# Kernel optimization log

Measured on AMD Instinct MI355X. Metric: run time of the kernel, lower is better.

The kernel has to match this reference:

```python
import jax, jax.numpy as jnp
import numpy as np

D_MODEL, D_STATE, D_CONV, D_INNER, DT_RANK = 1024, 16, 4, 2048, 64
B_SZ, L = 4, 2048

def setup_inputs() -> dict:
    key = jax.random.key(0)
    ks = jax.random.split(key, 7)
    return {
        "hidden_states": jax.random.normal(ks[0], (B_SZ, L, D_MODEL), jnp.float32),
        "in_proj_w": jax.random.normal(ks[1], (2 * D_INNER, D_MODEL), jnp.float32) * (D_MODEL ** -0.5),
        "conv_w": jax.random.normal(ks[2], (D_INNER, 1, D_CONV), jnp.float32) * 0.5,
        "conv_b": jax.random.normal(ks[3], (D_INNER,), jnp.float32) * 0.1,
        "x_proj_w": jax.random.normal(ks[4], (DT_RANK + 2 * D_STATE, D_INNER), jnp.float32) * (D_INNER ** -0.5),
        "dt_proj_w": jax.random.normal(ks[5], (D_INNER, DT_RANK), jnp.float32) * (DT_RANK ** -0.5),
        "A_log": jax.random.uniform(ks[6], (D_INNER, D_STATE), jnp.float32, 0.0, 2.0),
    }

def reference(hidden_states, in_proj_w, conv_w, conv_b, x_proj_w, dt_proj_w, A_log):
    b, l, d = hidden_states.shape
    # in_proj: (b,l,d) x (2*d_inner,d)^T -> (b, 2*d_inner, l)
    xz = jnp.einsum('bld,ed->bel', hidden_states, in_proj_w)
    x, z = jnp.split(xz, 2, axis=1)  # each (b, d_inner, l); z unused downstream
    A = -jnp.exp(A_log)              # (d_inner, d_state)
    # causal depthwise conv1d (left pad d_conv-1) + SiLU
    x = jax.lax.conv_general_dilated(
        x, conv_w, window_strides=(1,), padding=[(D_CONV - 1, 0)],
        feature_group_count=D_INNER,
        dimension_numbers=('NCH', 'OIH', 'NCH'))
    x = jax.nn.silu(x + conv_b[None, :, None])  # (b, d_inner, l)
    # x_proj: (b,l,dt_rank+2*d_state)
    x_dbl = jnp.einsum('bdl,ed->ble', x, x_proj_w)
    dt, B_mat, C_mat = jnp.split(x_dbl, [DT_RANK, DT_RANK + D_STATE], axis=-1)
    dt = jnp.einsum('blr,dr->bdl', dt, dt_proj_w)          # (b, d_inner, l), no bias
    B_mat = jnp.swapaxes(B_mat, 1, 2)                      # (b, d_state, l)
    C_mat = jnp.swapaxes(C_mat, 1, 2)                      # (b, d_state, l)
    return (dt, A, B_mat, C_mat, x)
```

## Files before the change

kernel.cpp:

```cpp
#include <hip/hip_runtime.h>
#include <hip/hip_bf16.h>
#include <math.h>

#define D_MODEL 1024
#define D_STATE 16
#define D_CONV  4
#define D_INNER 2048
#define DT_RANK 64
#define B_SZ    4
#define L_SEQ   2048

#define OFF_DT 0
#define OFF_A  (B_SZ * D_INNER * L_SEQ)
#define OFF_B  (OFF_A + D_INNER * D_STATE)
#define OFF_C  (OFF_B + B_SZ * D_STATE * L_SEQ)
#define OFF_X  (OFF_C + B_SZ * D_STATE * L_SEQ)

typedef __attribute__((ext_vector_type(8))) short bf16x8;
typedef __attribute__((ext_vector_type(8))) unsigned short us8;
typedef __attribute__((ext_vector_type(4))) float f32x4;
typedef unsigned short ushort_t;
typedef unsigned int uint_t;

static __device__ __forceinline__ ushort_t f2bf(float f) {
  __hip_bfloat16 h = __float2bfloat16(f);
  return *(ushort_t*)&h;
}
static __device__ __forceinline__ float bf2f(ushort_t u) {
  union { uint_t u; float f; } c;
  c.u = ((uint_t)u) << 16;
  return c.f;
}

#define N4_HS   (B_SZ * L_SEQ * D_MODEL / 4)
#define N4_W    (D_INNER * D_MODEL / 4)
#define N4_XW   ((DT_RANK + 2 * D_STATE) * D_INNER / 4)
#define N4_Z0   (B_SZ * DT_RANK * L_SEQ / 4)
#define N4_Z1   (2 * B_SZ * D_STATE * L_SEQ / 4)
#define N4_A    (D_INNER * D_STATE / 4)
#define N4_TOT  (N4_HS + N4_W + N4_XW + N4_Z0 + N4_Z1 + N4_A)

__global__ __launch_bounds__(256) void k_prep(
    const float4* __restrict__ hs, const float4* __restrict__ ipw,
    const float4* __restrict__ xpw, const float4* __restrict__ alog,
    ushort4* __restrict__ bfHS, ushort4* __restrict__ bfW,
    ushort4* __restrict__ xwb,
    float4* __restrict__ z0, float4* __restrict__ z1,
    float4* __restrict__ aout) {
  int i = blockIdx.x * 256 + threadIdx.x;
  if (i < N4_HS) {
    float4 v = hs[i];
    ushort4 o; o.x = f2bf(v.x); o.y = f2bf(v.y); o.z = f2bf(v.z); o.w = f2bf(v.w);
    bfHS[i] = o;
    return;
  }
  i -= N4_HS;
  if (i < N4_W) {
    float4 v = ipw[i];
    ushort4 o; o.x = f2bf(v.x); o.y = f2bf(v.y); o.z = f2bf(v.z); o.w = f2bf(v.w);
    bfW[i] = o;
    return;
  }
  i -= N4_W;
  if (i < N4_XW) {
    float4 v = xpw[i];
    ushort4 o; o.x = f2bf(v.x); o.y = f2bf(v.y); o.z = f2bf(v.z); o.w = f2bf(v.w);
    xwb[i] = o;
    return;
  }
  i -= N4_XW;
  if (i < N4_Z0) { z0[i] = (float4){0.f, 0.f, 0.f, 0.f}; return; }
  i -= N4_Z0;
  if (i < N4_Z1) { z1[i] = (float4){0.f, 0.f, 0.f, 0.f}; return; }
  i -= N4_Z1;
  if (i < N4_A) {
    float4 v = alog[i];
    float4 o;
    o.x = -expf(v.x); o.y = -expf(v.y); o.z = -expf(v.z); o.w = -expf(v.w);
    aout[i] = o;
  }
}

__global__ __launch_bounds__(256) void k_inproj_mfma(
    const ushort_t* __restrict__ Wb,
    const ushort_t* __restrict__ HSb,
    ushort_t* __restrict__ Cout) {
  const int flat = blockIdx.x + 16 * blockIdx.y + 256 * blockIdx.z;
  const int swz  = (flat & 7) * 128 + (flat >> 3);
  const int bn = swz & 15;
  const int bm = (swz >> 4) & 15;
  const int b  = swz >> 8;

  __shared__ ushort_t As[128 * 32];
  __shared__ ushort_t Bs[128 * 32];
  const int tid  = threadIdx.x;
  const int wv   = tid >> 6;
  const int lane = tid & 63;
  const int wr = wv >> 1, wc = wv & 1;

  const int srow = tid >> 2;
  const int ss   = tid & 3;

  const ushort_t* Ag = Wb + (size_t)(bm * 128) * D_MODEL;
  const ushort_t* Bg = HSb + (size_t)b * L_SEQ * D_MODEL
                           + (size_t)(bn * 128) * D_MODEL;

  f32x4 acc[4][4];
#pragma unroll
  for (int i = 0; i < 4; ++i)
#pragma unroll
    for (int j = 0; j < 4; ++j) acc[i][j] = (f32x4){0.f, 0.f, 0.f, 0.f};

  const int ksel = lane >> 4;
  const int frow = lane & 15;

  for (int k0 = 0; k0 < D_MODEL; k0 += 32) {
#pragma unroll
    for (int q = 0; q < 2; ++q) {
      int row = q * 64 + srow;
      int xs  = ss ^ ((row >> 1) & 3);
      const ushort_t* ga = Ag + (size_t)row * D_MODEL + k0 + xs * 8;
      const ushort_t* gb = Bg + (size_t)row * D_MODEL + k0 + xs * 8;
      ushort_t* la = As + (q * 256 + wv * 64) * 8;
      ushort_t* lb = Bs + (q * 256 + wv * 64) * 8;
      __builtin_amdgcn_global_load_lds((const __attribute__((address_space(1))) void*)ga,
                                       (__attribute__((address_space(3))) void*)la, 16, 0, 0);
      __builtin_amdgcn_global_load_lds((const __attribute__((address_space(1))) void*)gb,
                                       (__attribute__((address_space(3))) void*)lb, 16, 0, 0);
    }
    __syncthreads();

    bf16x8 af[4], bfr[4];
#pragma unroll
    for (int m = 0; m < 4; ++m) {
      int row = wr * 64 + m * 16 + frow;
      af[m] = *(const bf16x8*)(As + (row * 4 + (ksel ^ ((row >> 1) & 3))) * 8);
    }
#pragma unroll
    for (int n = 0; n < 4; ++n) {
      int row = wc * 64 + n * 16 + frow;
      bfr[n] = *(const bf16x8*)(Bs + (row * 4 + (ksel ^ ((row >> 1) & 3))) * 8);
    }
#pragma unroll
    for (int m = 0; m < 4; ++m)
#pragma unroll
      for (int n = 0; n < 4; ++n)
        acc[m][n] = __builtin_amdgcn_mfma_f32_16x16x32_bf16(af[m], bfr[n], acc[m][n], 0, 0, 0);
    __syncthreads();
  }

  const int crow0 = (lane >> 4) * 4;
  const int ccol  = lane & 15;
  ushort_t* Cb = Cout + (size_t)b * D_INNER * L_SEQ;
#pragma unroll
  for (int m = 0; m < 4; ++m) {
    int gr0 = bm * 128 + wr * 64 + m * 16 + crow0;
#pragma unroll
    for (int n = 0; n < 4; ++n) {
      int gc = bn * 128 + wc * 64 + n * 16 + ccol;
#pragma unroll
      for (int i = 0; i < 4; ++i)
        Cb[(size_t)(gr0 + i) * L_SEQ + gc] = f2bf(acc[m][n][i]);
    }
  }
}

__global__ __launch_bounds__(256) void k_conv(const ushort_t* __restrict__ Xp,
                                              const float* __restrict__ CW,
                                              const float* __restrict__ CB,
                                              float* __restrict__ Xo) {
  const int bd = blockIdx.x;
  const int d  = bd & (D_INNER - 1);
  const ushort_t* row = Xp + (size_t)bd * L_SEQ;
  float* orow = Xo + (size_t)bd * L_SEQ;
  const float w0 = CW[d * 4 + 0], w1 = CW[d * 4 + 1];
  const float w2 = CW[d * 4 + 2], w3 = CW[d * 4 + 3];
  const float bias = CB[d];
  const int l0 = threadIdx.x << 3;

  us8 cur = *(const us8*)(row + l0);
  float e[11];
  e[0] = 0.f; e[1] = 0.f; e[2] = 0.f;
  if (l0 >= 4) {
    ushort4 pv = *(const ushort4*)(row + l0 - 4);
    e[0] = bf2f(pv.y); e[1] = bf2f(pv.z); e[2] = bf2f(pv.w);
  }
#pragma unroll
  for (int j = 0; j < 8; ++j) e[3 + j] = bf2f(cur[j]);

  float4 o0, o1;
  float* op = &o0.x;
#pragma unroll
  for (int j = 0; j < 8; ++j) {
    float v = w0 * e[j] + w1 * e[j + 1] + w2 * e[j + 2] + w3 * e[j + 3] + bias;
    float s = v / (1.f + expf(-v));
    if (j < 4) (&o0.x)[j] = s; else (&o1.x)[j - 4] = s;
  }
  (void)op;
  *(float4*)(orow + l0)     = o0;
  *(float4*)(orow + l0 + 4) = o1;
}

__global__ __launch_bounds__(256) void k_xproj_mfma(
    const ushort_t* __restrict__ XWb,
    const float* __restrict__ X,
    float* __restrict__ XDBL,
    float* __restrict__ OutB,
    float* __restrict__ OutC) {
  const int ln = blockIdx.x;
  const int sk = blockIdx.y;
  const int b  = blockIdx.z;
  __shared__ ushort_t As[96 * 40];
  __shared__ ushort_t Bs[128 * 34];
  const int tid  = threadIdx.x;
  const int wv   = tid >> 6;
  const int lane = tid & 63;
  const int wr = wv >> 1, wc = wv & 1;
  const int ksel = lane >> 4;
  const int frow = lane & 15;

  const float* Xb = X + (size_t)b * D_INNER * L_SEQ + (size_t)ln * 128;

  f32x4 acc[3][4];
#pragma unroll
  for (int i = 0; i < 3; ++i)
#pragma unroll
    for (int j = 0; j < 4; ++j) acc[i][j] = (f32x4){0.f, 0.f, 0.f, 0.f};

  for (int k0 = 0; k0 < 256; k0 += 32) {
    const int koff = sk * 256 + k0;
    {
      int row = tid >> 2, s = tid & 3;
      bf16x8 v = *(const bf16x8*)(XWb + (size_t)row * D_INNER + koff + s * 8);
      *(bf16x8*)(As + row * 40 + s * 8) = v;
      if (tid < 128) {
        int row2 = 64 + (tid >> 2);
        bf16x8 v2 = *(const bf16x8*)(XWb + (size_t)row2 * D_INNER + koff + s * 8);
        *(bf16x8*)(As + row2 * 40 + s * 8) = v2;
      }
    }
#pragma unroll
    for (int j = 0; j < 2; ++j) {
      int u = tid + 256 * j;
      int n4 = u & 31;
      int kp = u >> 5;
      const float* g0 = Xb + (size_t)(koff + 2 * kp) * L_SEQ + 4 * n4;
      float4 x0 = *(const float4*)g0;
      float4 x1 = *(const float4*)(g0 + L_SEQ);
      float e0[4] = {x0.x, x0.y, x0.z, x0.w};
      float e1[4] = {x1.x, x1.y, x1.z, x1.w};
#pragma unroll
      for (int i = 0; i < 4; ++i) {
        uint_t pk = (uint_t)f2bf(e0[i]) | ((uint_t)f2bf(e1[i]) << 16);
        int n = 4 * n4 + i;
        *(uint_t*)(Bs + n * 34 + 2 * kp) = pk;
      }
    }
    __syncthreads();

    bf16x8 af[3], bfr[4];
#pragma unroll
    for (int mi = 0; mi < 3; ++mi) {
      int row = wr * 48 + mi * 16 + frow;
      af[mi] = *(const bf16x8*)(As + row * 40 + ksel * 8);
    }
#pragma unroll
    for (int ni = 0; ni < 4; ++ni) {
      int n = wc * 64 + ni * 16 + frow;
      const uint_t* p = (const uint_t*)(Bs + n * 34);
      union { uint_t u[4]; bf16x8 v; } fr;
#pragma unroll
      for (int q = 0; q < 4; ++q) fr.u[q] = p[ksel * 4 + q];
      bfr[ni] = fr.v;
    }
#pragma unroll
    for (int mi = 0; mi < 3; ++mi)
#pragma unroll
      for (int ni = 0; ni < 4; ++ni)
        acc[mi][ni] = __builtin_amdgcn_mfma_f32_16x16x32_bf16(af[mi], bfr[ni], acc[mi][ni], 0, 0, 0);
    __syncthreads();
  }

  const int crow0 = (lane >> 4) * 4;
  const int ccol  = lane & 15;
#pragma unroll
  for (int mi = 0; mi < 3; ++mi) {
    int e0 = wr * 48 + mi * 16 + crow0;
    float* base;
    int eoff;
    if (e0 < 64)      { base = XDBL + (size_t)b * 64 * L_SEQ; eoff = e0; }
    else if (e0 < 80) { base = OutB + (size_t)b * D_STATE * L_SEQ; eoff = e0 - 64; }
    else              { base = OutC + (size_t)b * D_STATE * L_SEQ; eoff = e0 - 80; }
#pragma unroll
    for (int ni = 0; ni < 4; ++ni) {
      int l = ln * 128 + wc * 64 + ni * 16 + ccol;
#pragma unroll
      for (int r = 0; r < 4; ++r)
        atomicAdd(base + (size_t)(eoff + r) * L_SEQ + l, acc[mi][ni][r]);
    }
  }
}

__global__ __launch_bounds__(256) void k_dt(const float* __restrict__ DW,
                                            const float* __restrict__ XDBL,
                                            float* __restrict__ DT) {
  const int b = blockIdx.z, bm = blockIdx.y, bn = blockIdx.x;
  __shared__ float As[64][68];
  __shared__ float Bs[64][68];
  const int tid = threadIdx.x;
  const int tx = tid & 15, ty = tid >> 4;
  const int row = tid >> 4;
  const int col = (tid & 15) << 2;
  const float* Bb = XDBL + (size_t)b * DT_RANK * L_SEQ;
#pragma unroll
  for (int q = 0; q < 4; ++q) {
    int r = q * 16 + row;
    float4 av = *(const float4*)(DW + (size_t)(bm * 64 + r) * DT_RANK + col);
    As[col + 0][r] = av.x; As[col + 1][r] = av.y;
    As[col + 2][r] = av.z; As[col + 3][r] = av.w;
    float4 bv = *(const float4*)(Bb + (size_t)r * L_SEQ + bn * 64 + col);
    *(float4*)&Bs[r][col] = bv;
  }
  __syncthreads();
  float acc[4][4] = {};
#pragma unroll 16
  for (int kk = 0; kk < 64; ++kk) {
    float4 a4 = *(const float4*)&As[kk][ty << 2];
    float4 b4 = *(const float4*)&Bs[kk][tx << 2];
    float a[4] = {a4.x, a4.y, a4.z, a4.w};
    float bb[4] = {b4.x, b4.y, b4.z, b4.w};
#pragma unroll
    for (int i = 0; i < 4; ++i)
#pragma unroll
      for (int j = 0; j < 4; ++j) acc[i][j] += a[i] * bb[j];
  }
  float* Cp = DT + (size_t)b * D_INNER * L_SEQ
                 + (size_t)(bm * 64 + (ty << 2)) * L_SEQ + bn * 64 + (tx << 2);
#pragma unroll
  for (int i = 0; i < 4; ++i) {
    float4 v = make_float4(acc[i][0], acc[i][1], acc[i][2], acc[i][3]);
    *(float4*)(Cp + (size_t)i * L_SEQ) = v;
  }
}

extern "C" void kernel_launch(void* const* d_in, const int* in_sizes, int n_in,
                              void* d_out, int out_size, void* d_ws, size_t ws_size,
                              hipStream_t stream) {
  const float* hs   = (const float*)d_in[0];
  const float* ipw  = (const float*)d_in[1];
  const float* cw   = (const float*)d_in[2];
  const float* cb   = (const float*)d_in[3];
  const float* xpw  = (const float*)d_in[4];
  const float* dpw  = (const float*)d_in[5];
  const float* alog = (const float*)d_in[6];

  float* out    = (float*)d_out;
  float* dt_out = out + OFF_DT;
  float* a_out  = out + OFF_A;
  float* b_out  = out + OFF_B;
  float* c_out  = out + OFF_C;
  float* x_out  = out + OFF_X;

  unsigned short* bfHS = (unsigned short*)x_out;
  unsigned short* bfW  = bfHS + (size_t)B_SZ * L_SEQ * D_MODEL;
  unsigned short* xpre = (unsigned short*)dt_out;
  float* xdbl = (float*)d_ws;
  unsigned short* xwb = (unsigned short*)((char*)d_ws + (size_t)B_SZ * DT_RANK * L_SEQ * 4);

  k_prep<<<dim3(N4_TOT / 256), 256, 0, stream>>>(
      (const float4*)hs, (const float4*)ipw, (const float4*)xpw,
      (const float4*)alog,
      (ushort4*)bfHS, (ushort4*)bfW, (ushort4*)xwb,
      (float4*)xdbl, (float4*)b_out, (float4*)a_out);

  k_inproj_mfma<<<dim3(16, 16, 4), 256, 0, stream>>>(bfW, bfHS, xpre);
  k_conv<<<dim3(B_SZ * D_INNER), 256, 0, stream>>>(xpre, cw, cb, x_out);
  k_xproj_mfma<<<dim3(16, 8, 4), 256, 0, stream>>>(xwb, x_out, xdbl, b_out, c_out);
  k_dt<<<dim3(32, 32, 4), 256, 0, stream>>>(dpw, xdbl, dt_out);
}
```

Measured before the change: 149.4 us.

## Fuse causal conv+SiLU into x_proj GEMM and move dt_proj to bf16 MFMA

The standalone conv kernel is removed. The x_proj GEMM now loads the bf16 pre-conv activations, applies the depthwise causal conv, bias and SiLU in its tile loader, writes the fp32 x output, and feeds the bf16 result straight into LDS. This avoids reading the full fp32 x tensor back and saves a launch. The fp32 SIMT dt_proj GEMM is replaced by a bf16 MFMA kernel on 128x128 tiles, with the weight converted to bf16 in the prep kernel. The trade-off is lower dt precision and scalar per-lane output stores in place of the earlier float4 stores.

```diff
diff --git a/kernel.cpp b/kernel.cpp
--- a/kernel.cpp
+++ b/kernel.cpp
@@ -35,16 +35,18 @@
 #define N4_HS   (B_SZ * L_SEQ * D_MODEL / 4)
 #define N4_W    (D_INNER * D_MODEL / 4)
 #define N4_XW   ((DT_RANK + 2 * D_STATE) * D_INNER / 4)
+#define N4_DW   (D_INNER * DT_RANK / 4)
 #define N4_Z0   (B_SZ * DT_RANK * L_SEQ / 4)
 #define N4_Z1   (2 * B_SZ * D_STATE * L_SEQ / 4)
 #define N4_A    (D_INNER * D_STATE / 4)
-#define N4_TOT  (N4_HS + N4_W + N4_XW + N4_Z0 + N4_Z1 + N4_A)
+#define N4_TOT  (N4_HS + N4_W + N4_XW + N4_DW + N4_Z0 + N4_Z1 + N4_A)
 
 __global__ __launch_bounds__(256) void k_prep(
     const float4* __restrict__ hs, const float4* __restrict__ ipw,
-    const float4* __restrict__ xpw, const float4* __restrict__ alog,
+    const float4* __restrict__ xpw, const float4* __restrict__ dpw,
+    const float4* __restrict__ alog,
     ushort4* __restrict__ bfHS, ushort4* __restrict__ bfW,
-    ushort4* __restrict__ xwb,
+    ushort4* __restrict__ xwb, ushort4* __restrict__ dwb,
     float4* __restrict__ z0, float4* __restrict__ z1,
     float4* __restrict__ aout) {
   int i = blockIdx.x * 256 + threadIdx.x;
@@ -69,6 +71,13 @@
     return;
   }
   i -= N4_XW;
+  if (i < N4_DW) {
+    float4 v = dpw[i];
+    ushort4 o; o.x = f2bf(v.x); o.y = f2bf(v.y); o.z = f2bf(v.z); o.w = f2bf(v.w);
+    dwb[i] = o;
+    return;
+  }
+  i -= N4_DW;
   if (i < N4_Z0) { z0[i] = (float4){0.f, 0.f, 0.f, 0.f}; return; }
   i -= N4_Z0;
   if (i < N4_Z1) { z1[i] = (float4){0.f, 0.f, 0.f, 0.f}; return; }
@@ -165,45 +174,12 @@
   }
 }
 
-__global__ __launch_bounds__(256) void k_conv(const ushort_t* __restrict__ Xp,
-                                              const float* __restrict__ CW,
-                                              const float* __restrict__ CB,
-                                              float* __restrict__ Xo) {
-  const int bd = blockIdx.x;
-  const int d  = bd & (D_INNER - 1);
-  const ushort_t* row = Xp + (size_t)bd * L_SEQ;
-  float* orow = Xo + (size_t)bd * L_SEQ;
-  const float w0 = CW[d * 4 + 0], w1 = CW[d * 4 + 1];
-  const float w2 = CW[d * 4 + 2], w3 = CW[d * 4 + 3];
-  const float bias = CB[d];
-  const int l0 = threadIdx.x << 3;
-
-  us8 cur = *(const us8*)(row + l0);
-  float e[11];
-  e[0] = 0.f; e[1] = 0.f; e[2] = 0.f;
-  if (l0 >= 4) {
-    ushort4 pv = *(const ushort4*)(row + l0 - 4);
-    e[0] = bf2f(pv.y); e[1] = bf2f(pv.z); e[2] = bf2f(pv.w);
-  }
-#pragma unroll
-  for (int j = 0; j < 8; ++j) e[3 + j] = bf2f(cur[j]);
-
-  float4 o0, o1;
-  float* op = &o0.x;
-#pragma unroll
-  for (int j = 0; j < 8; ++j) {
-    float v = w0 * e[j] + w1 * e[j + 1] + w2 * e[j + 2] + w3 * e[j + 3] + bias;
-    float s = v / (1.f + expf(-v));
-    if (j < 4) (&o0.x)[j] = s; else (&o1.x)[j - 4] = s;
-  }
-  (void)op;
-  *(float4*)(orow + l0)     = o0;
-  *(float4*)(orow + l0 + 4) = o1;
-}
-
-__global__ __launch_bounds__(256) void k_xproj_mfma(
+__global__ __launch_bounds__(256) void k_xproj_fused(
     const ushort_t* __restrict__ XWb,
-    const float* __restrict__ X,
+    const ushort_t* __restrict__ Xpre,
+    const float* __restrict__ CW,
+    const float* __restrict__ CB,
+    float* __restrict__ Xout,
     float* __restrict__ XDBL,
     float* __restrict__ OutB,
     float* __restrict__ OutC) {
@@ -219,8 +195,6 @@
   const int ksel = lane >> 4;
   const int frow = lane & 15;
 
-  const float* Xb = X + (size_t)b * D_INNER * L_SEQ + (size_t)ln * 128;
-
   f32x4 acc[3][4];
 #pragma unroll
   for (int i = 0; i < 3; ++i)
@@ -244,16 +218,33 @@
       int u = tid + 256 * j;
       int n4 = u & 31;
       int kp = u >> 5;
-      const float* g0 = Xb + (size_t)(koff + 2 * kp) * L_SEQ + 4 * n4;
-      float4 x0 = *(const float4*)g0;
-      float4 x1 = *(const float4*)(g0 + L_SEQ);
-      float e0[4] = {x0.x, x0.y, x0.z, x0.w};
-      float e1[4] = {x1.x, x1.y, x1.z, x1.w};
+      int l0 = ln * 128 + 4 * n4;
+      float sv[2][4];
+#pragma unroll
+      for (int r = 0; r < 2; ++r) {
+        int d = koff + 2 * kp + r;
+        const ushort_t* row = Xpre + ((size_t)b * D_INNER + d) * L_SEQ;
+        ushort4 cur = *(const ushort4*)(row + l0);
+        float em3 = 0.f, em2 = 0.f, em1 = 0.f;
+        if (l0 >= 4) {
+          ushort4 pv = *(const ushort4*)(row + l0 - 4);
+          em3 = bf2f(pv.y); em2 = bf2f(pv.z); em1 = bf2f(pv.w);
+        }
+        float ee[7] = {em3, em2, em1, bf2f(cur.x), bf2f(cur.y), bf2f(cur.z), bf2f(cur.w)};
+        float4 w = *(const float4*)(CW + d * 4);
+        float bias = CB[d];
+#pragma unroll
+        for (int i = 0; i < 4; ++i) {
+          float v = w.x * ee[i] + w.y * ee[i + 1] + w.z * ee[i + 2] + w.w * ee[i + 3] + bias;
+          sv[r][i] = v / (1.f + expf(-v));
+        }
+        *(float4*)(Xout + ((size_t)b * D_INNER + d) * L_SEQ + l0) =
+            make_float4(sv[r][0], sv[r][1], sv[r][2], sv[r][3]);
+      }
 #pragma unroll
       for (int i = 0; i < 4; ++i) {
-        uint_t pk = (uint_t)f2bf(e0[i]) | ((uint_t)f2bf(e1[i]) << 16);
-        int n = 4 * n4 + i;
-        *(uint_t*)(Bs + n * 34 + 2 * kp) = pk;
+        uint_t pk = (uint_t)f2bf(sv[0][i]) | ((uint_t)f2bf(sv[1][i]) << 16);
+        *(uint_t*)(Bs + (4 * n4 + i) * 34 + 2 * kp) = pk;
       }
     }
     __syncthreads();
@@ -301,45 +292,86 @@
   }
 }
 
-__global__ __launch_bounds__(256) void k_dt(const float* __restrict__ DW,
-                                            const float* __restrict__ XDBL,
-                                            float* __restrict__ DT) {
-  const int b = blockIdx.z, bm = blockIdx.y, bn = blockIdx.x;
-  __shared__ float As[64][68];
-  __shared__ float Bs[64][68];
-  const int tid = threadIdx.x;
-  const int tx = tid & 15, ty = tid >> 4;
-  const int row = tid >> 4;
-  const int col = (tid & 15) << 2;
-  const float* Bb = XDBL + (size_t)b * DT_RANK * L_SEQ;
+__global__ __launch_bounds__(256) void k_dt_mfma(
+    const ushort_t* __restrict__ DWb,
+    const float* __restrict__ XDBL,
+    float* __restrict__ DT) {
+  const int ln = blockIdx.x;
+  const int dm = blockIdx.y;
+  const int b  = blockIdx.z;
+  __shared__ ushort_t As[128 * 72];
+  __shared__ ushort_t Bs[128 * 68];
+  const int tid  = threadIdx.x;
+  const int wv   = tid >> 6;
+  const int lane = tid & 63;
+  const int wr = wv >> 1, wc = wv & 1;
+  const int ksel = lane >> 4;
+  const int frow = lane & 15;
+
 #pragma unroll
   for (int q = 0; q < 4; ++q) {
-    int r = q * 16 + row;
-    float4 av = *(const float4*)(DW + (size_t)(bm * 64 + r) * DT_RANK + col);
-    As[col + 0][r] = av.x; As[col + 1][r] = av.y;
-    As[col + 2][r] = av.z; As[col + 3][r] = av.w;
-    float4 bv = *(const float4*)(Bb + (size_t)r * L_SEQ + bn * 64 + col);
-    *(float4*)&Bs[r][col] = bv;
+    int u = tid + 256 * q;
+    int row = u >> 3, s = u & 7;
+    *(bf16x8*)(As + row * 72 + s * 8) =
+        *(const bf16x8*)(DWb + (size_t)(dm * 128 + row) * DT_RANK + s * 8);
+  }
+#pragma unroll
+  for (int q = 0; q < 4; ++q) {
+    int u = tid + 256 * q;
+    int n4 = u & 31;
+    int kp = u >> 5;
+    const float* g = XDBL + ((size_t)b * DT_RANK + 2 * kp) * L_SEQ + ln * 128 + 4 * n4;
+    float4 x0 = *(const float4*)g;
+    float4 x1 = *(const float4*)(g + L_SEQ);
+    float e0[4] = {x0.x, x0.y, x0.z, x0.w};
+    float e1[4] = {x1.x, x1.y, x1.z, x1.w};
+#pragma unroll
+    for (int i = 0; i < 4; ++i) {
+      uint_t pk = (uint_t)f2bf(e0[i]) | ((uint_t)f2bf(e1[i]) << 16);
+      *(uint_t*)(Bs + (4 * n4 + i) * 68 + 2 * kp) = pk;
+    }
   }
   __syncthreads();
-  float acc[4][4] = {};
-#pragma unroll 16
-  for (int kk = 0; kk < 64; ++kk) {
-    float4 a4 = *(const float4*)&As[kk][ty << 2];
-    float4 b4 = *(const float4*)&Bs[kk][tx << 2];
-    float a[4] = {a4.x, a4.y, a4.z, a4.w};
-    float bb[4] = {b4.x, b4.y, b4.z, b4.w};
-#pragma unroll
-    for (int i = 0; i < 4; ++i)
-#pragma unroll
-      for (int j = 0; j < 4; ++j) acc[i][j] += a[i] * bb[j];
-  }
-  float* Cp = DT + (size_t)b * D_INNER * L_SEQ
-                 + (size_t)(bm * 64 + (ty << 2)) * L_SEQ + bn * 64 + (tx << 2);
-#pragma unroll
-  for (int i = 0; i < 4; ++i) {
-    float4 v = make_float4(acc[i][0], acc[i][1], acc[i][2], acc[i][3]);
-    *(float4*)(Cp + (size_t)i * L_SEQ) = v;
+
+  f32x4 acc[4][4];
+#pragma unroll
+  for (int i = 0; i < 4; ++i)
+#pragma unroll
+    for (int j = 0; j < 4; ++j) acc[i][j] = (f32x4){0.f, 0.f, 0.f, 0.f};
+
+#pragma unroll
+  for (int ks = 0; ks < 2; ++ks) {
+    bf16x8 af[4], bfr[4];
+#pragma unroll
+    for (int m = 0; m < 4; ++m) {
+      int row = wr * 64 + m * 16 + frow;
+      af[m] = *(const bf16x8*)(As + row * 72 + ks * 32 + ksel * 8);
+    }
+#pragma unroll
+    for (int n = 0; n < 4; ++n) {
+      int nn = wc * 64 + n * 16 + frow;
+      bfr[n] = *(const bf16x8*)(Bs + nn * 68 + ks * 32 + ksel * 8);
+    }
+#pragma unroll
+    for (int m = 0; m < 4; ++m)
+#pragma unroll
+      for (int n = 0; n < 4; ++n)
+        acc[m][n] = __builtin_amdgcn_mfma_f32_16x16x32_bf16(af[m], bfr[n], acc[m][n], 0, 0, 0);
+  }
+
+  const int crow0 = (lane >> 4) * 4;
+  const int ccol  = lane & 15;
+  float* Cb = DT + (size_t)b * D_INNER * L_SEQ;
+#pragma unroll
+  for (int m = 0; m < 4; ++m) {
+    int gr0 = dm * 128 + wr * 64 + m * 16 + crow0;
+#pragma unroll
+    for (int n = 0; n < 4; ++n) {
+      int gc = ln * 128 + wc * 64 + n * 16 + ccol;
+#pragma unroll
+      for (int i = 0; i < 4; ++i)
+        Cb[(size_t)(gr0 + i) * L_SEQ + gc] = acc[m][n][i];
+    }
   }
 }
 
@@ -365,16 +397,17 @@
   unsigned short* bfW  = bfHS + (size_t)B_SZ * L_SEQ * D_MODEL;
   unsigned short* xpre = (unsigned short*)dt_out;
   float* xdbl = (float*)d_ws;
-  unsigned short* xwb = (unsigned short*)((char*)d_ws + (size_t)B_SZ * DT_RANK * L_SEQ * 4);
-
-  k_prep<<<dim3(N4_TOT / 256), 256, 0, stream>>>(
+  unsigned short* xwb = (unsigned short*)((char*)d_ws + 2097152);
+  unsigned short* dwb = (unsigned short*)((char*)d_ws + 2097152 + 393216);
+
+  k_prep<<<dim3((N4_TOT + 255) / 256), 256, 0, stream>>>(
       (const float4*)hs, (const float4*)ipw, (const float4*)xpw,
-      (const float4*)alog,
-      (ushort4*)bfHS, (ushort4*)bfW, (ushort4*)xwb,
+      (const float4*)dpw, (const float4*)alog,
+      (ushort4*)bfHS, (ushort4*)bfW, (ushort4*)xwb, (ushort4*)dwb,
       (float4*)xdbl, (float4*)b_out, (float4*)a_out);
 
   k_inproj_mfma<<<dim3(16, 16, 4), 256, 0, stream>>>(bfW, bfHS, xpre);
-  k_conv<<<dim3(B_SZ * D_INNER), 256, 0, stream>>>(xpre, cw, cb, x_out);
-  k_xproj_mfma<<<dim3(16, 8, 4), 256, 0, stream>>>(xwb, x_out, xdbl, b_out, c_out);
-  k_dt<<<dim3(32, 32, 4), 256, 0, stream>>>(dpw, xdbl, dt_out);
-}
+  k_xproj_fused<<<dim3(16, 8, 4), 256, 0, stream>>>(xwb, xpre, cw, cb,
+                                                    x_out, xdbl, b_out, c_out);
+  k_dt_mfma<<<dim3(16, 16, 4), 256, 0, stream>>>(dwb, xdbl, dt_out);
+}
```

Result: faster. 133.0 us (-11.0%).
